# Kernel tuning notes

Hardware: AMD Instinct MI355X
Metric: run time of the kernel (lower is better)

The kernel has to match this reference:

```python
import jax, jax.numpy as jnp
import numpy as np

H = 256      # hidden_dim
NH = 4       # num_heads (fixed in __init__)


def _mha_pool(x, mask, Wqkv, bqkv, Wo, bo):
    """Batched torch-style MultiheadAttention (self-attn) + masked mean pool.
    x: [..., L, H], mask: [..., L] float {0,1} (1 = valid).
    Returns pooled embedding [..., H]. Fully-masked rows yield zeros
    (numerator is 0, denominator is 1e-10), matching the torch branch.
    """
    h = x.shape[-1]
    dh = h // NH
    qkv = x @ Wqkv.T + bqkv                      # [..., L, 3H]
    q, k, v = jnp.split(qkv, 3, axis=-1)
    split = lambda t: t.reshape(t.shape[:-1] + (NH, dh))
    q, k, v = split(q), split(k), split(v)
    scale = 1.0 / jnp.sqrt(jnp.asarray(dh, x.dtype))
    scores = jnp.einsum('...qhd,...khd->...hqk', q, k) * scale
    # key_padding_mask: masked keys get large negative logit
    scores = scores + (1.0 - mask)[..., None, None, :] * jnp.asarray(-1e9, x.dtype)
    attn = jax.nn.softmax(scores, axis=-1)
    o = jnp.einsum('...hqk,...khd->...qhd', attn, v)
    o = o.reshape(o.shape[:-2] + (h,)) @ Wo.T + bo   # out_proj
    pooled = (o * mask[..., None]).sum(-2) / (mask.sum(-1, keepdims=True) + 1e-10)
    return pooled


def _mha_params(key):
    k1, k2 = jax.random.split(key)
    s = 1.0 / np.sqrt(H)
    Wqkv = jax.random.uniform(k1, (3 * H, H), jnp.float32, -s, s)
    bqkv = jnp.zeros((3 * H,), jnp.float32)
    Wo = jax.random.uniform(k2, (H, H), jnp.float32, -s, s)
    bo = jnp.zeros((H,), jnp.float32)
    return Wqkv, bqkv, Wo, bo


def setup_inputs() -> dict:
    key = jax.random.key(0)
    k0, k1, kw, ks, kc = jax.random.split(key, 5)
    B, SEC, SEN, W = 16, 8, 16, 64
    we = jax.random.normal(k0, (B, SEC, SEN, W, H), jnp.float32)
    am = jax.random.randint(k1, (B, SEC, SEN, W), 0, 2, jnp.int32)
    wW, wb, wO, wob = _mha_params(kw)
    sW, sb, sO, sob = _mha_params(ks)
    cW, cb, cO, cob = _mha_params(kc)
    return {
        'word_embeddings': we, 'attention_mask': am,
        'word_Wqkv': wW, 'word_bqkv': wb, 'word_Wo': wO, 'word_bo': wob,
        'sent_Wqkv': sW, 'sent_bqkv': sb, 'sent_Wo': sO, 'sent_bo': sob,
        'sect_Wqkv': cW, 'sect_bqkv': cb, 'sect_Wo': cO, 'sect_bo': cob,
    }


def reference(word_embeddings, attention_mask,
              word_Wqkv, word_bqkv, word_Wo, word_bo,
              sent_Wqkv, sent_bqkv, sent_Wo, sent_bo,
              sect_Wqkv, sect_bqkv, sect_Wo, sect_bo):
    wm = attention_mask.astype(word_embeddings.dtype)            # [B,Sec,Sen,W]
    # word level -> sentence embeddings [B,Sec,Sen,H]
    sent = _mha_pool(word_embeddings, wm, word_Wqkv, word_bqkv, word_Wo, word_bo)
    # sentence level -> section embeddings [B,Sec,H]
    sm = (wm.sum(-1) > 0).astype(word_embeddings.dtype)          # [B,Sec,Sen]
    sect = _mha_pool(sent, sm, sent_Wqkv, sent_bqkv, sent_Wo, sent_bo)
    # section level -> doc embeddings [B,H]
    cm = (wm.sum((-1, -2)) > 0).astype(word_embeddings.dtype)    # [B,Sec]
    doc = _mha_pool(sect, cm, sect_Wqkv, sect_bqkv, sect_Wo, sect_bo)
    return doc
```

## Files before the change

kernel.cpp:

```cpp
#include <hip/hip_runtime.h>
#include <hip/hip_bf16.h>


typedef short bf16x8 __attribute__((ext_vector_type(8)));
typedef float f32x4 __attribute__((ext_vector_type(4)));
typedef unsigned int u32x4 __attribute__((ext_vector_type(4)));
typedef unsigned short U16;
typedef unsigned int U32;

__device__ __forceinline__ U16 f2bf(float f) {
    __hip_bfloat16 b = __float2bfloat16(f);
    return __builtin_bit_cast(U16, b);
}
__device__ __forceinline__ void split_hl(float f, U16& h, U16& l) {
    h = f2bf(f);
    float hf = __builtin_bit_cast(float, (U32)h << 16);
    l = f2bf(f - hf);
}

#define MFMA(A, B, C) __builtin_amdgcn_mfma_f32_16x16x32_bf16( \
    __builtin_bit_cast(bf16x8, A), __builtin_bit_cast(bf16x8, B), C, 0, 0, 0)

template <int RS, int SW>
__device__ __forceinline__ u32x4 fragp(const U16* base, int row, int k, int lhi) {
    int slot = ((k >> 3) + lhi) ^ (row & SW);
    return *(const u32x4*)(base + row * RS + slot * 8);
}
template <int RS, int SW>
__device__ __forceinline__ void put16(U16* base, int row, int col, U16 v) {
    int slot = (col >> 3) ^ (row & SW);
    base[row * RS + slot * 8 + (col & 7)] = v;
}
template <int RS, int SW>
__device__ __forceinline__ void put64(U16* base, int row, int col0,
                                      U16 v0, U16 v1, U16 v2, U16 v3) {
    int slot = (col0 >> 3) ^ (row & SW);
    U32* p = (U32*)(base + row * RS + slot * 8 + (col0 & 7));
    p[0] = (U32)v0 | ((U32)v1 << 16);
    p[1] = (U32)v2 | ((U32)v3 << 16);
}

__device__ __forceinline__ void stage8(U16* ph, U16* pl, int row, int c8,
                                       float4 a, float4 b) {
    U16 h[8], l[8];
    split_hl(a.x, h[0], l[0]); split_hl(a.y, h[1], l[1]);
    split_hl(a.z, h[2], l[2]); split_hl(a.w, h[3], l[3]);
    split_hl(b.x, h[4], l[4]); split_hl(b.y, h[5], l[5]);
    split_hl(b.z, h[6], l[6]); split_hl(b.w, h[7], l[7]);
    u32x4 hv, lv;
    #pragma unroll
    for (int q = 0; q < 4; ++q) {
        hv[q] = (U32)h[2*q] | ((U32)h[2*q+1] << 16);
        lv[q] = (U32)l[2*q] | ((U32)l[2*q+1] << 16);
    }
    const int slot = c8 ^ (row & 7);
    *(u32x4*)(ph + row * 64 + slot * 8) = hv;
    *(u32x4*)(pl + row * 64 + slot * 8) = lv;
}

__global__ __launch_bounds__(256) void convert_w(
    const float* __restrict__ Wq, const float* __restrict__ Wo,
    U16* __restrict__ qh, U16* __restrict__ ql,
    U16* __restrict__ oh, U16* __restrict__ ol)
{
    int i = blockIdx.x * 256 + threadIdx.x;
    if (i < 768 * 256) { U16 h, l; split_hl(Wq[i], h, l); qh[i] = h; ql[i] = l; }
    if (i < 256 * 256) { U16 h, l; split_hl(Wo[i], h, l); oh[i] = h; ol[i] = l; }
}

__global__ __launch_bounds__(256, 2) void word_mfma(
    const float* __restrict__ x, const int* __restrict__ am,
    const U16* __restrict__ Wqh, const U16* __restrict__ Wql,
    const float* __restrict__ bqkv,
    const float* __restrict__ Wo32,
    const float* __restrict__ bo,
    U16* __restrict__ sent_hi, U16* __restrict__ sent_lo,
    float* __restrict__ smask)
{
    __shared__ __align__(16) U16 QsH[64 * 64], QsL[64 * 64];
    __shared__ __align__(16) U16 KsH[64 * 64], KsL[64 * 64];
    __shared__ __align__(16) U16 VXH[64 * 64], VXL[64 * 64];
    __shared__ float msk[64];
    __shared__ float smsum;

    const int t = threadIdx.x;
    const int w = t >> 6, l = t & 63, l15 = l & 15, lhi = l >> 4;
    const int b = blockIdx.x;
    const float* xb = x + (size_t)b * 16384;

    if (t < 64) msk[t] = (float)am[b * 64 + t];

    const int r0 = t >> 3, c8 = t & 7;
    const int r1 = r0 + 32;

    float po[16];

    #pragma unroll 1
    for (int h = 0; h < 4; ++h) {
        float4 s00 = *(const float4*)(xb + r0 * 256 + c8 * 8);
        float4 s01 = *(const float4*)(xb + r0 * 256 + c8 * 8 + 4);
        float4 s10 = *(const float4*)(xb + r1 * 256 + c8 * 8);
        float4 s11 = *(const float4*)(xb + r1 * 256 + c8 * 8 + 4);
        f32x4 acc[3][4];
        #pragma unroll
        for (int j = 0; j < 3; ++j)
            #pragma unroll
            for (int mt = 0; mt < 4; ++mt) acc[j][mt] = f32x4{0.f, 0.f, 0.f, 0.f};

        for (int kc = 0; kc < 4; ++kc) {
            __syncthreads();
            stage8(VXH, VXL, r0, c8, s00, s01);
            stage8(VXH, VXL, r1, c8, s10, s11);
            __syncthreads();
            if (kc < 3) {
                s00 = *(const float4*)(xb + r0 * 256 + (kc + 1) * 64 + c8 * 8);
                s01 = *(const float4*)(xb + r0 * 256 + (kc + 1) * 64 + c8 * 8 + 4);
                s10 = *(const float4*)(xb + r1 * 256 + (kc + 1) * 64 + c8 * 8);
                s11 = *(const float4*)(xb + r1 * 256 + (kc + 1) * 64 + c8 * 8 + 4);
            }
            #pragma unroll
            for (int ks = 0; ks < 2; ++ks) {
                const int kt = ks * 32;
                const int kk = kc * 64 + kt + lhi * 8;
                const size_t wr0 = (size_t)(          h * 64 + w * 16 + l15) * 256 + kk;
                const size_t wr1 = (size_t)(256     + h * 64 + w * 16 + l15) * 256 + kk;
                const size_t wr2 = (size_t)(512     + h * 64 + w * 16 + l15) * 256 + kk;
                u32x4 wh0 = *(const u32x4*)(Wqh + wr0);
                u32x4 wl0 = *(const u32x4*)(Wql + wr0);
                u32x4 wh1 = *(const u32x4*)(Wqh + wr1);
                u32x4 wl1 = *(const u32x4*)(Wql + wr1);
                u32x4 wh2 = *(const u32x4*)(Wqh + wr2);
                u32x4 wl2 = *(const u32x4*)(Wql + wr2);
                #pragma unroll
                for (int mt = 0; mt < 4; ++mt) {
                    u32x4 xh = fragp<64, 7>(VXH, mt * 16 + l15, kt, lhi);
                    u32x4 xl = fragp<64, 7>(VXL, mt * 16 + l15, kt, lhi);
                    acc[0][mt] = MFMA(xh, wh0, acc[0][mt]);
                    acc[0][mt] = MFMA(xh, wl0, acc[0][mt]);
                    acc[0][mt] = MFMA(xl, wh0, acc[0][mt]);
                    acc[1][mt] = MFMA(xh, wh1, acc[1][mt]);
                    acc[1][mt] = MFMA(xh, wl1, acc[1][mt]);
                    acc[1][mt] = MFMA(xl, wh1, acc[1][mt]);
                    acc[2][mt] = MFMA(xh, wh2, acc[2][mt]);
                    acc[2][mt] = MFMA(xh, wl2, acc[2][mt]);
                    acc[2][mt] = MFMA(xl, wh2, acc[2][mt]);
                }
            }
        }
        {
            const float bQ = bqkv[      h * 64 + w * 16 + l15];
            const float bK = bqkv[256 + h * 64 + w * 16 + l15];
            #pragma unroll
            for (int mt = 0; mt < 4; ++mt) {
                #pragma unroll
                for (int r = 0; r < 4; ++r) {
                    U16 vH, vL;
                    split_hl(acc[0][mt][r] + bQ, vH, vL);
                    put16<64, 7>(QsH, mt * 16 + lhi * 4 + r, w * 16 + l15, vH);
                    put16<64, 7>(QsL, mt * 16 + lhi * 4 + r, w * 16 + l15, vL);
                    split_hl(acc[1][mt][r] + bK, vH, vL);
                    put16<64, 7>(KsH, mt * 16 + lhi * 4 + r, w * 16 + l15, vH);
                    put16<64, 7>(KsL, mt * 16 + lhi * 4 + r, w * 16 + l15, vL);
                }
            }
        }
        __syncthreads();
        {
            const float bV = bqkv[512 + h * 64 + w * 16 + l15];
            const int d = w * 16 + l15;
            #pragma unroll
            for (int mt = 0; mt < 4; ++mt) {
                U16 h4[4], l4[4];
                #pragma unroll
                for (int r = 0; r < 4; ++r)
                    split_hl(acc[2][mt][r] + bV, h4[r], l4[r]);
                put64<64, 7>(VXH, d, mt * 16 + lhi * 4, h4[0], h4[1], h4[2], h4[3]);
                put64<64, 7>(VXL, d, mt * 16 + lhi * 4, l4[0], l4[1], l4[2], l4[3]);
            }
        }
        __syncthreads();
        if (h == 0 && t == 0) {
            float s = 0.f;
            for (int i = 0; i < 64; ++i) s += msk[i];
            smsum = s;
        }

        {
            f32x4 sa[4];
            #pragma unroll
            for (int i = 0; i < 4; ++i) sa[i] = f32x4{0.f, 0.f, 0.f, 0.f};
            #pragma unroll
            for (int ks = 0; ks < 2; ++ks) {
                const int kt = ks * 32;
                u32x4 qh = fragp<64, 7>(QsH, w * 16 + l15, kt, lhi);
                u32x4 ql = fragp<64, 7>(QsL, w * 16 + l15, kt, lhi);
                #pragma unroll
                for (int nt = 0; nt < 4; ++nt) {
                    u32x4 kh = fragp<64, 7>(KsH, nt * 16 + l15, kt, lhi);
                    u32x4 kl = fragp<64, 7>(KsL, nt * 16 + l15, kt, lhi);
                    sa[nt] = MFMA(qh, kh, sa[nt]);
                    sa[nt] = MFMA(qh, kl, sa[nt]);
                    sa[nt] = MFMA(ql, kh, sa[nt]);
                }
            }
            float sc[4][4];
            #pragma unroll
            for (int nt = 0; nt < 4; ++nt) {
                const float mterm = (1.0f - msk[nt * 16 + l15]) * -1e9f;
                #pragma unroll
                for (int r = 0; r < 4; ++r) sc[nt][r] = sa[nt][r] * 0.125f + mterm;
            }
            #pragma unroll
            for (int r = 0; r < 4; ++r) {
                float m = fmaxf(fmaxf(sc[0][r], sc[1][r]), fmaxf(sc[2][r], sc[3][r]));
                #pragma unroll
                for (int off = 1; off < 16; off <<= 1) m = fmaxf(m, __shfl_xor(m, off));
                float e0 = expf(sc[0][r] - m), e1 = expf(sc[1][r] - m);
                float e2 = expf(sc[2][r] - m), e3 = expf(sc[3][r] - m);
                float s = e0 + e1 + e2 + e3;
                #pragma unroll
                for (int off = 1; off < 16; off <<= 1) s += __shfl_xor(s, off);
                const float inv = 1.0f / s;
                sc[0][r] = e0 * inv; sc[1][r] = e1 * inv;
                sc[2][r] = e2 * inv; sc[3][r] = e3 * inv;
            }
            #pragma unroll
            for (int nt = 0; nt < 4; ++nt) {
                #pragma unroll
                for (int r = 0; r < 4; ++r) {
                    U16 vH, vL; split_hl(sc[nt][r], vH, vL);
                    put16<64, 7>(QsH, w * 16 + lhi * 4 + r, nt * 16 + l15, vH);
                    put16<64, 7>(QsL, w * 16 + lhi * 4 + r, nt * 16 + l15, vL);
                }
            }
        }
        {
            f32x4 pa[4];
            #pragma unroll
            for (int i = 0; i < 4; ++i) pa[i] = f32x4{0.f, 0.f, 0.f, 0.f};
            #pragma unroll
            for (int ks = 0; ks < 2; ++ks) {
                const int kt = ks * 32;
                u32x4 ph = fragp<64, 7>(QsH, w * 16 + l15, kt, lhi);
                u32x4 pl = fragp<64, 7>(QsL, w * 16 + l15, kt, lhi);
                #pragma unroll
                for (int nt = 0; nt < 4; ++nt) {
                    u32x4 vh = fragp<64, 7>(VXH, nt * 16 + l15, kt, lhi);
                    u32x4 vl = fragp<64, 7>(VXL, nt * 16 + l15, kt, lhi);
                    pa[nt] = MFMA(ph, vh, pa[nt]);
                    pa[nt] = MFMA(ph, vl, pa[nt]);
                    pa[nt] = MFMA(pl, vh, pa[nt]);
                }
            }
            float sarr[4];
            #pragma unroll
            for (int nt = 0; nt < 4; ++nt) {
                float s = 0.f;
                #pragma unroll
                for (int r = 0; r < 4; ++r)
                    s += msk[w * 16 + lhi * 4 + r] * pa[nt][r];
                s += __shfl_xor(s, 16);
                s += __shfl_xor(s, 32);
                sarr[nt] = s;
            }
            if (h == 0) {
                po[0] = sarr[0]; po[1] = sarr[1]; po[2] = sarr[2]; po[3] = sarr[3];
            } else if (h == 1) {
                po[4] = sarr[0]; po[5] = sarr[1]; po[6] = sarr[2]; po[7] = sarr[3];
            } else if (h == 2) {
                po[8] = sarr[0]; po[9] = sarr[1]; po[10] = sarr[2]; po[11] = sarr[3];
            } else {
                po[12] = sarr[0]; po[13] = sarr[1]; po[14] = sarr[2]; po[15] = sarr[3];
            }
        }
    }

    __syncthreads();
    float (*part)[256] = (float(*)[256])KsH;
    if (lhi == 0) {
        #pragma unroll
        for (int hh = 0; hh < 4; ++hh)
            #pragma unroll
            for (int nt = 0; nt < 4; ++nt)
                part[w][hh * 64 + nt * 16 + l15] = po[hh * 4 + nt];
    }
    __syncthreads();
    {
        float opv = part[0][t] + part[1][t] + part[2][t] + part[3][t];
        part[0][t] = opv;
    }
    __syncthreads();
    {
        const float* wrow = Wo32 + (size_t)t * 256;
        const float* opool = part[0];
        float s = 0.f;
        #pragma unroll 8
        for (int c = 0; c < 256; c += 4) {
            float4 wv = *(const float4*)(wrow + c);
            s += opool[c] * wv.x + opool[c + 1] * wv.y
               + opool[c + 2] * wv.z + opool[c + 3] * wv.w;
        }
        float m = smsum;
        float val = (s + bo[t] * m) / (m + 1e-10f);
        U16 vH, vL; split_hl(val, vH, vL);
        sent_hi[(size_t)b * 256 + t] = vH;
        sent_lo[(size_t)b * 256 + t] = vL;
    }
    if (t == 0) smask[b] = (smsum > 0.f) ? 1.f : 0.f;
}

template <int L>
__global__ __launch_bounds__(256) void mha_small(
    const U16* __restrict__ xh, const U16* __restrict__ xl,
    const float* __restrict__ mk,
    const U16* __restrict__ Wqh, const U16* __restrict__ Wql,
    const float* __restrict__ bqkv,
    const U16* __restrict__ Woh, const U16* __restrict__ Wol,
    const float* __restrict__ bo,
    float* __restrict__ out_f32, U16* __restrict__ out_hi, U16* __restrict__ out_lo,
    float* __restrict__ outmask)
{
    __shared__ __align__(16) U16 xs_h[16*256], xs_l[16*256];
    __shared__ __align__(16) U16 Qh_[16*256], Ql_[16*256];
    __shared__ __align__(16) U16 Kh_[16*256], Kl_[16*256];
    __shared__ __align__(16) U16 Vh_[256*32], Vl_[256*32];
    __shared__ __align__(16) U16 Ph_[4][16*32], Pl_[4][16*32];
    __shared__ __align__(16) U16 Oh_[16*256], Ol_[16*256];
    __shared__ float msk[16];
    __shared__ float smsum;

    const int t = threadIdx.x;
    const int w = t >> 6, l = t & 63, l15 = l & 15, lhi = l >> 4;
    const int b = blockIdx.x;

    if (t < 16) msk[t] = (t < L) ? mk[b*L + t] : 0.f;

    #pragma unroll
    for (int i = 0; i < 2; ++i) {
        int c = i*256 + t;
        int row = c >> 5, c8 = c & 31;
        u32x4 hv = u32x4{0,0,0,0}, lv = u32x4{0,0,0,0};
        if (row < L) {
            hv = *(const u32x4*)(xh + ((size_t)b*L + row)*256 + c8*8);
            lv = *(const u32x4*)(xl + ((size_t)b*L + row)*256 + c8*8);
        }
        int slot = c8 ^ (row & 7);
        *(u32x4*)(xs_h + row*256 + slot*8) = hv;
        *(u32x4*)(xs_l + row*256 + slot*8) = lv;
    }
    #pragma unroll
    for (int i = 0; i < 4; ++i) {
        int c = i*256 + t;
        *(u32x4*)(Vh_ + c*8) = u32x4{0,0,0,0};
        *(u32x4*)(Vl_ + c*8) = u32x4{0,0,0,0};
    }
    *(u32x4*)(&Ph_[0][0] + t*8) = u32x4{0,0,0,0};
    *(u32x4*)(&Pl_[0][0] + t*8) = u32x4{0,0,0,0};
    __syncthreads();
    if (t == 0) { float s = 0.f; for (int i = 0; i < 16; ++i) s += msk[i]; smsum = s; }

    {
        f32x4 acc[12];
        #pragma unroll
        for (int i = 0; i < 12; ++i) acc[i] = f32x4{0.f,0.f,0.f,0.f};
        #pragma unroll 2
        for (int k0 = 0; k0 < 256; k0 += 32) {
            u32x4 ah = fragp<256,7>(xs_h, l15, k0, lhi);
            u32x4 al = fragp<256,7>(xs_l, l15, k0, lhi);
            #pragma unroll
            for (int j = 0; j < 12; ++j) {
                int u = w*12 + j;
                u32x4 wh = *(const u32x4*)(Wqh + (size_t)(u*16 + l15)*256 + k0 + lhi*8);
                u32x4 wl = *(const u32x4*)(Wql + (size_t)(u*16 + l15)*256 + k0 + lhi*8);
                acc[j] = MFMA(ah, wh, acc[j]);
                acc[j] = MFMA(ah, wl, acc[j]);
                acc[j] = MFMA(al, wh, acc[j]);
            }
        }
        #pragma unroll
        for (int j = 0; j < 12; ++j) {
            int u = w*12 + j;
            int mat = u >> 4, cg = u & 15;
            float bias = bqkv[u*16 + l15];
            if (mat < 2) {
                U16* dh = (mat == 0) ? Qh_ : Kh_;
                U16* dl = (mat == 0) ? Ql_ : Kl_;
                #pragma unroll
                for (int r = 0; r < 4; ++r) {
                    U16 vH, vL; split_hl(acc[j][r] + bias, vH, vL);
                    put16<256,7>(dh, lhi*4 + r, cg*16 + l15, vH);
                    put16<256,7>(dl, lhi*4 + r, cg*16 + l15, vL);
                }
            } else {
                U16 h4[4], l4[4];
                #pragma unroll
                for (int r = 0; r < 4; ++r) split_hl(acc[j][r] + bias, h4[r], l4[r]);
                put64<32,3>(Vh_, cg*16 + l15, lhi*4, h4[0],h4[1],h4[2],h4[3]);
                put64<32,3>(Vl_, cg*16 + l15, lhi*4, l4[0],l4[1],l4[2],l4[3]);
            }
        }
    }
    __syncthreads();

    {
        const int h = w;
        f32x4 sa = f32x4{0.f,0.f,0.f,0.f};
        #pragma unroll
        for (int k0 = 0; k0 < 64; k0 += 32) {
            u32x4 qh = fragp<256,7>(Qh_, l15, h*64 + k0, lhi);
            u32x4 ql = fragp<256,7>(Ql_, l15, h*64 + k0, lhi);
            u32x4 kh = fragp<256,7>(Kh_, l15, h*64 + k0, lhi);
            u32x4 kl = fragp<256,7>(Kl_, l15, h*64 + k0, lhi);
            sa = MFMA(qh, kh, sa);
            sa = MFMA(qh, kl, sa);
            sa = MFMA(ql, kh, sa);
        }
        float sc[4];
        float mterm = (1.0f - msk[l15]) * -1e9f;
        #pragma unroll
        for (int r = 0; r < 4; ++r) sc[r] = sa[r] * 0.125f + mterm;
        #pragma unroll
        for (int r = 0; r < 4; ++r) {
            float m = sc[r];
            #pragma unroll
            for (int off = 1; off < 16; off <<= 1) m = fmaxf(m, __shfl_xor(m, off));
            float e = expf(sc[r] - m);
            float s = e;
            #pragma unroll
            for (int off = 1; off < 16; off <<= 1) s += __shfl_xor(s, off);
            sc[r] = e / s;
        }
        #pragma unroll
        for (int r = 0; r < 4; ++r) {
            U16 vH, vL; split_hl(sc[r], vH, vL);
            put16<32,3>(&Ph_[h][0], lhi*4 + r, l15, vH);
            put16<32,3>(&Pl_[h][0], lhi*4 + r, l15, vL);
        }
        f32x4 pa[4];
        #pragma unroll
        for (int i = 0; i < 4; ++i) pa[i] = f32x4{0.f,0.f,0.f,0.f};
        {
            u32x4 ph = fragp<32,3>(&Ph_[h][0], l15, 0, lhi);
            u32x4 pl = fragp<32,3>(&Pl_[h][0], l15, 0, lhi);
            #pragma unroll
            for (int ntl = 0; ntl < 4; ++ntl) {
                u32x4 vh = fragp<32,3>(Vh_, h*64 + ntl*16 + l15, 0, lhi);
                u32x4 vl = fragp<32,3>(Vl_, h*64 + ntl*16 + l15, 0, lhi);
                pa[ntl] = MFMA(ph, vh, pa[ntl]);
                pa[ntl] = MFMA(ph, vl, pa[ntl]);
                pa[ntl] = MFMA(pl, vh, pa[ntl]);
            }
        }
        #pragma unroll
        for (int ntl = 0; ntl < 4; ++ntl) {
            #pragma unroll
            for (int r = 0; r < 4; ++r) {
                U16 vH, vL; split_hl(pa[ntl][r], vH, vL);
                put16<256,7>(Oh_, lhi*4 + r, h*64 + ntl*16 + l15, vH);
                put16<256,7>(Ol_, lhi*4 + r, h*64 + ntl*16 + l15, vL);
            }
        }
    }
    __syncthreads();

    {
        f32x4 acc4[4];
        #pragma unroll
        for (int i = 0; i < 4; ++i) acc4[i] = f32x4{0.f,0.f,0.f,0.f};
        #pragma unroll 2
        for (int k0 = 0; k0 < 256; k0 += 32) {
            u32x4 oh = fragp<256,7>(Oh_, l15, k0, lhi);
            u32x4 ol = fragp<256,7>(Ol_, l15, k0, lhi);
            #pragma unroll
            for (int j = 0; j < 4; ++j) {
                int oc = w*64 + j*16 + l15;
                u32x4 wh = *(const u32x4*)(Woh + (size_t)oc*256 + k0 + lhi*8);
                u32x4 wl = *(const u32x4*)(Wol + (size_t)oc*256 + k0 + lhi*8);
                acc4[j] = MFMA(oh, wh, acc4[j]);
                acc4[j] = MFMA(oh, wl, acc4[j]);
                acc4[j] = MFMA(ol, wh, acc4[j]);
            }
        }
        float msum = smsum;
        #pragma unroll
        for (int j = 0; j < 4; ++j) {
            float s = 0.f;
            #pragma unroll
            for (int r = 0; r < 4; ++r) s += msk[lhi*4 + r] * acc4[j][r];
            s += __shfl_xor(s, 16);
            s += __shfl_xor(s, 32);
            if (lhi == 0) {
                int col = w*64 + j*16 + l15;
                float val = (s + bo[col] * msum) / (msum + 1e-10f);
                if (out_f32) out_f32[(size_t)b*256 + col] = val;
                if (out_hi) {
                    U16 vH, vL; split_hl(val, vH, vL);
                    out_hi[(size_t)b*256 + col] = vH;
                    out_lo[(size_t)b*256 + col] = vL;
                }
            }
        }
    }
    if (t == 0 && outmask) outmask[b] = (smsum > 0.f) ? 1.f : 0.f;
}

extern "C" void kernel_launch(void* const* d_in, const int* in_sizes, int n_in,
                              void* d_out, int out_size, void* d_ws, size_t ws_size,
                              hipStream_t stream) {
    (void)in_sizes; (void)n_in; (void)out_size; (void)ws_size;
    const float* we  = (const float*)d_in[0];
    const int*   am  = (const int*)d_in[1];
    const float* wW  = (const float*)d_in[2];
    const float* wb  = (const float*)d_in[3];
    const float* wO  = (const float*)d_in[4];
    const float* wob = (const float*)d_in[5];
    const float* sW  = (const float*)d_in[6];
    const float* sb  = (const float*)d_in[7];
    const float* sO  = (const float*)d_in[8];
    const float* sob = (const float*)d_in[9];
    const float* cW  = (const float*)d_in[10];
    const float* cb  = (const float*)d_in[11];
    const float* cO  = (const float*)d_in[12];
    const float* cob = (const float*)d_in[13];

    U16* p = (U16*)d_ws;
    U16* sent_hi = p; p += 2048*256;
    U16* sent_lo = p; p += 2048*256;
    U16* sect_hi = p; p += 128*256;
    U16* sect_lo = p; p += 128*256;
    U16* w1qh = p; p += 768*256;  U16* w1ql = p; p += 768*256;
    U16* w1oh = p; p += 256*256;  U16* w1ol = p; p += 256*256;
    U16* w2qh = p; p += 768*256;  U16* w2ql = p; p += 768*256;
    U16* w2oh = p; p += 256*256;  U16* w2ol = p; p += 256*256;
    U16* w3qh = p; p += 768*256;  U16* w3ql = p; p += 768*256;
    U16* w3oh = p; p += 256*256;  U16* w3ol = p; p += 256*256;
    float* smaskb = (float*)p;
    float* cmaskb = smaskb + 2048;

    convert_w<<<768, 256, 0, stream>>>(wW, wO, w1qh, w1ql, w1oh, w1ol);
    convert_w<<<768, 256, 0, stream>>>(sW, sO, w2qh, w2ql, w2oh, w2ol);
    convert_w<<<768, 256, 0, stream>>>(cW, cO, w3qh, w3ql, w3oh, w3ol);
    word_mfma<<<2048, 256, 0, stream>>>(we, am, w1qh, w1ql, wb, wO, wob,
                                        sent_hi, sent_lo, smaskb);
    mha_small<16><<<128, 256, 0, stream>>>(sent_hi, sent_lo, smaskb,
                                           w2qh, w2ql, sb, w2oh, w2ol, sob,
                                           nullptr, sect_hi, sect_lo, cmaskb);
    mha_small<8><<<16, 256, 0, stream>>>(sect_hi, sect_lo, cmaskb,
                                         w3qh, w3ql, cb, w3oh, w3ol, cob,
                                         (float*)d_out, nullptr, nullptr, nullptr);
}
```

Baseline: 414.9 us.

## Double-buffer X staging in LDS to overlap loads with QKV MFMA

Replaces the single X staging buffer with two ping-pong LDS buffers. Each k-chunk is loaded from global memory and split to bf16 hi/lo while the previous chunk feeds the MFMAs, which removes one barrier per chunk and merges the Q/K and V write-out phases. The first chunk of the next head is prefetched across the head loop, and the V tile now reuses the second X buffer. This adds 16 KB of LDS, which may reduce occupancy below the two blocks per CU the launch bounds request.

Result: slower. 544.8 us (+31.3%).

```diff
diff --git a/kernel.cpp b/kernel.cpp
--- a/kernel.cpp
+++ b/kernel.cpp
@@ -79,7 +79,8 @@
 {
     __shared__ __align__(16) U16 QsH[64 * 64], QsL[64 * 64];
     __shared__ __align__(16) U16 KsH[64 * 64], KsL[64 * 64];
-    __shared__ __align__(16) U16 VXH[64 * 64], VXL[64 * 64];
+    __shared__ __align__(16) U16 XAH[64 * 64], XAL[64 * 64];
+    __shared__ __align__(16) U16 XBH[64 * 64], XBL[64 * 64];
     __shared__ float msk[64];
     __shared__ float smsum;
 
@@ -93,30 +94,40 @@
     const int r0 = t >> 3, c8 = t & 7;
     const int r1 = r0 + 32;
 
-    float po[16];
-
-    #pragma unroll 1
-    for (int h = 0; h < 4; ++h) {
+    {
         float4 s00 = *(const float4*)(xb + r0 * 256 + c8 * 8);
         float4 s01 = *(const float4*)(xb + r0 * 256 + c8 * 8 + 4);
         float4 s10 = *(const float4*)(xb + r1 * 256 + c8 * 8);
         float4 s11 = *(const float4*)(xb + r1 * 256 + c8 * 8 + 4);
+        stage8(XAH, XAL, r0, c8, s00, s01);
+        stage8(XAH, XAL, r1, c8, s10, s11);
+    }
+
+    float po[16];
+
+    #pragma unroll 1
+    for (int h = 0; h < 4; ++h) {
+        __syncthreads();
         f32x4 acc[3][4];
         #pragma unroll
         for (int j = 0; j < 3; ++j)
             #pragma unroll
             for (int mt = 0; mt < 4; ++mt) acc[j][mt] = f32x4{0.f, 0.f, 0.f, 0.f};
 
+        #pragma unroll
         for (int kc = 0; kc < 4; ++kc) {
-            __syncthreads();
-            stage8(VXH, VXL, r0, c8, s00, s01);
-            stage8(VXH, VXL, r1, c8, s10, s11);
-            __syncthreads();
-            if (kc < 3) {
-                s00 = *(const float4*)(xb + r0 * 256 + (kc + 1) * 64 + c8 * 8);
-                s01 = *(const float4*)(xb + r0 * 256 + (kc + 1) * 64 + c8 * 8 + 4);
-                s10 = *(const float4*)(xb + r1 * 256 + (kc + 1) * 64 + c8 * 8);
-                s11 = *(const float4*)(xb + r1 * 256 + (kc + 1) * 64 + c8 * 8 + 4);
+            const U16* xph = (kc & 1) ? XBH : XAH;
+            const U16* xpl = (kc & 1) ? XBL : XAL;
+            U16* sth = (kc & 1) ? XAH : XBH;
+            U16* stl = (kc & 1) ? XAL : XBL;
+            const int ck = ((kc + 1) & 3) * 64;
+            const bool doStage = (kc < 3) || (h < 3);
+            float4 s00, s01, s10, s11;
+            if (doStage) {
+                s00 = *(const float4*)(xb + r0 * 256 + ck + c8 * 8);
+                s01 = *(const float4*)(xb + r0 * 256 + ck + c8 * 8 + 4);
+                s10 = *(const float4*)(xb + r1 * 256 + ck + c8 * 8);
+                s11 = *(const float4*)(xb + r1 * 256 + ck + c8 * 8 + 4);
             }
             #pragma unroll
             for (int ks = 0; ks < 2; ++ks) {
@@ -133,8 +144,8 @@
                 u32x4 wl2 = *(const u32x4*)(Wql + wr2);
                 #pragma unroll
                 for (int mt = 0; mt < 4; ++mt) {
-                    u32x4 xh = fragp<64, 7>(VXH, mt * 16 + l15, kt, lhi);
-                    u32x4 xl = fragp<64, 7>(VXL, mt * 16 + l15, kt, lhi);
+                    u32x4 xh = fragp<64, 7>(xph, mt * 16 + l15, kt, lhi);
+                    u32x4 xl = fragp<64, 7>(xpl, mt * 16 + l15, kt, lhi);
                     acc[0][mt] = MFMA(xh, wh0, acc[0][mt]);
                     acc[0][mt] = MFMA(xh, wl0, acc[0][mt]);
                     acc[0][mt] = MFMA(xl, wh0, acc[0][mt]);
@@ -146,6 +157,11 @@
                     acc[2][mt] = MFMA(xl, wh2, acc[2][mt]);
                 }
             }
+            if (doStage) {
+                stage8(sth, stl, r0, c8, s00, s01);
+                stage8(sth, stl, r1, c8, s10, s11);
+            }
+            __syncthreads();
         }
         {
             const float bQ = bqkv[      h * 64 + w * 16 + l15];
@@ -163,9 +179,6 @@
                     put16<64, 7>(KsL, mt * 16 + lhi * 4 + r, w * 16 + l15, vL);
                 }
             }
-        }
-        __syncthreads();
-        {
             const float bV = bqkv[512 + h * 64 + w * 16 + l15];
             const int d = w * 16 + l15;
             #pragma unroll
@@ -174,8 +187,8 @@
                 #pragma unroll
                 for (int r = 0; r < 4; ++r)
                     split_hl(acc[2][mt][r] + bV, h4[r], l4[r]);
-                put64<64, 7>(VXH, d, mt * 16 + lhi * 4, h4[0], h4[1], h4[2], h4[3]);
-                put64<64, 7>(VXL, d, mt * 16 + lhi * 4, l4[0], l4[1], l4[2], l4[3]);
+                put64<64, 7>(XBH, d, mt * 16 + lhi * 4, h4[0], h4[1], h4[2], h4[3]);
+                put64<64, 7>(XBL, d, mt * 16 + lhi * 4, l4[0], l4[1], l4[2], l4[3]);
             }
         }
         __syncthreads();
@@ -245,8 +258,8 @@
                 u32x4 pl = fragp<64, 7>(QsL, w * 16 + l15, kt, lhi);
                 #pragma unroll
                 for (int nt = 0; nt < 4; ++nt) {
-                    u32x4 vh = fragp<64, 7>(VXH, nt * 16 + l15, kt, lhi);
-                    u32x4 vl = fragp<64, 7>(VXL, nt * 16 + l15, kt, lhi);
+                    u32x4 vh = fragp<64, 7>(XBH, nt * 16 + l15, kt, lhi);
+                    u32x4 vl = fragp<64, 7>(XBL, nt * 16 + l15, kt, lhi);
                     pa[nt] = MFMA(ph, vh, pa[nt]);
                     pa[nt] = MFMA(ph, vl, pa[nt]);
                     pa[nt] = MFMA(pl, vh, pa[nt]);
```
